# Kernel tuning notes

Hardware: AMD Instinct MI355X
Metric: run time of the kernel (lower is better)

The kernel has to match this reference:

```python
import jax, jax.numpy as jnp
import numpy as np

SCALE = 8.0  # sqrt(head_dim=64)


def setup_inputs() -> dict:
    key = jax.random.key(0)
    k1, k2, k3, k4 = jax.random.split(key, 4)
    B, Lq, Lk, H, C, K = 2, 4096, 4096, 8, 64, 32
    return {
        "query": jax.random.normal(k1, (B, Lq, H, C), dtype=jnp.float32),
        "key": jax.random.normal(k2, (B, Lk, H, C), dtype=jnp.float32),
        "value": jax.random.normal(k3, (B, Lk, H, C), dtype=jnp.float32),
        "pos": jax.random.randint(k4, (B, Lq, H, K), 0, Lk, dtype=jnp.int64),
    }


def reference(query, key, value, pos):
    # query: [B, Lq, H, C]; key/value: [B, Lk, H, C]; pos: [B, Lq, H, K]
    B, Lq, H, C = query.shape
    b_idx = jnp.arange(B)[:, None, None, None]   # [B,1,1,1]
    h_idx = jnp.arange(H)[None, None, :, None]   # [1,1,H,1]
    # gather along sequence dim per (batch, head): -> [B, Lq, H, K, C]
    k = key[b_idx, pos, h_idx, :]
    v = value[b_idx, pos, h_idx, :]
    # per-query attention over K gathered keys
    score = jnp.einsum("blhc,blhkc->blhk", query, k) / SCALE
    attn = jax.nn.softmax(score, axis=-1)
    out = jnp.einsum("blhk,blhkc->blhc", attn, v)
    return out
```

## Files before the change

### kernel.cpp

```cpp
#include <hip/hip_runtime.h>
#include <math.h>

constexpr int B  = 2;
constexpr int Lq = 4096;
constexpr int Lk = 4096;
constexpr int H  = 8;
constexpr int C  = 64;
constexpr int K  = 32;
constexpr float INV_SCALE = 0.125f;
constexpr int HC = H * C;
constexpr int NKV = B * Lk * H * C;

typedef _Float16 h2 __attribute__((ext_vector_type(2)));
typedef _Float16 half4_t __attribute__((ext_vector_type(4)));

static __device__ __forceinline__ h2 pack_h2(float lo, float hi) {
    return __builtin_bit_cast(h2, __builtin_amdgcn_cvt_pkrtz(lo, hi));
}

#if __has_builtin(__builtin_amdgcn_fdot2)
static __device__ __forceinline__ float fdot2(h2 a, h2 b, float c) {
    return __builtin_amdgcn_fdot2(a, b, c, false);
}
#else
static __device__ __forceinline__ float fdot2(h2 a, h2 b, float c) {
    return c + (float)a.x * (float)b.x + (float)a.y * (float)b.y;
}
#endif

static __device__ __forceinline__ h2 shfl_h2_xor(h2 v, int m) {
    int i = __builtin_bit_cast(int, v);
    i = __shfl_xor(i, m);
    return __builtin_bit_cast(h2, i);
}

template<int CTRL>
static __device__ __forceinline__ float dpp_f(float x) {
    return __builtin_bit_cast(float,
        __builtin_amdgcn_update_dpp(0, __builtin_bit_cast(int, x),
                                    CTRL, 0xF, 0xF, true));
}
template<int CTRL>
static __device__ __forceinline__ h2 dpp_h2(h2 x) {
    return __builtin_bit_cast(h2,
        __builtin_amdgcn_update_dpp(0, __builtin_bit_cast(int, x),
                                    CTRL, 0xF, 0xF, true));
}

__global__ __launch_bounds__(256) void convert_kv_f16(
    const float* __restrict__ key,
    const float* __restrict__ value,
    _Float16*    __restrict__ kh,
    _Float16*    __restrict__ vh)
{
    const int n4 = NKV / 4;
    for (int i = blockIdx.x * blockDim.x + threadIdx.x;
         i < 2 * n4; i += gridDim.x * blockDim.x) {
        if (i < n4) {
            const float4 v = ((const float4*)key)[i];
            half4_t h = { (_Float16)v.x, (_Float16)v.y, (_Float16)v.z, (_Float16)v.w };
            ((half4_t*)kh)[i] = h;
        } else {
            const float4 v = ((const float4*)value)[i - n4];
            half4_t h = { (_Float16)v.x, (_Float16)v.y, (_Float16)v.z, (_Float16)v.w };
            ((half4_t*)vh)[i - n4] = h;
        }
    }
}

__global__ __launch_bounds__(256, 2) void topk_attn_f16(
    const float*    __restrict__ query,
    const _Float16* __restrict__ keyh,
    const _Float16* __restrict__ valh,
    const int*      __restrict__ pos,
    float*          __restrict__ out)
{
    const int bid    = blockIdx.x;
    const int group  = bid & 15;
    const int lchunk = bid >> 4;
    const int wave   = threadIdx.x >> 6;
    const int lane   = threadIdx.x & 63;
    const int g      = lane >> 3;
    const int c8     = lane & 7;

    const int b = group >> 3;
    const int h = group & 7;
    const int l = lchunk * 4 + wave;

    const size_t row  = ((size_t)(b * Lq + l) * H + h);
    const size_t qoff = row * (size_t)C;

    const int4 pq = *(const int4*)(pos + row * (size_t)K + 4 * g);

    const _Float16* kbase = keyh + (size_t)b * Lk * HC + (size_t)h * C;
    const _Float16* vbase = valh + (size_t)b * Lk * HC + (size_t)h * C;

    int off[4];
    off[0] = pq.x * HC + 8 * c8;
    off[1] = pq.y * HC + 8 * c8;
    off[2] = pq.z * HC + 8 * c8;
    off[3] = pq.w * HC + 8 * c8;

    uint4 kv[4], vv[4];
    #pragma unroll
    for (int i = 0; i < 4; ++i) kv[i] = *(const uint4*)(kbase + off[i]);
    #pragma unroll
    for (int i = 0; i < 4; ++i) vv[i] = *(const uint4*)(vbase + off[i]);

    const float4 qa = *(const float4*)(query + qoff + 8 * c8);
    const float4 qb = *(const float4*)(query + qoff + 8 * c8 + 4);
    h2 qp[4];
    qp[0] = pack_h2(qa.x * INV_SCALE, qa.y * INV_SCALE);
    qp[1] = pack_h2(qa.z * INV_SCALE, qa.w * INV_SCALE);
    qp[2] = pack_h2(qb.x * INV_SCALE, qb.y * INV_SCALE);
    qp[3] = pack_h2(qb.z * INV_SCALE, qb.w * INV_SCALE);

    float s[4];
    #pragma unroll
    for (int i = 0; i < 4; ++i) {
        float t = fdot2(qp[0], __builtin_bit_cast(h2, kv[i].x), 0.0f);
        t = fdot2(qp[1], __builtin_bit_cast(h2, kv[i].y), t);
        t = fdot2(qp[2], __builtin_bit_cast(h2, kv[i].z), t);
        t = fdot2(qp[3], __builtin_bit_cast(h2, kv[i].w), t);
        t += dpp_f<0xB1>(t);
        t += dpp_f<0x4E>(t);
        t += dpp_f<0x141>(t);
        s[i] = t;
    }

    #pragma unroll
    for (int i = 0; i < 4; ++i) s[i] = __expf(s[i]);
    float se = (s[0] + s[1]) + (s[2] + s[3]);
    se += dpp_f<0x111>(se);
    se += dpp_f<0x112>(se);
    se += dpp_f<0x114>(se);
    se += dpp_f<0x118>(se);
    se += dpp_f<0x142>(se);
    se += dpp_f<0x143>(se);
    const float se_tot = __builtin_bit_cast(float,
        __builtin_amdgcn_readlane(__builtin_bit_cast(int, se), 63));
    const float inv = 8.0f / se_tot;

    h2 acc[4] = { h2{0,0}, h2{0,0}, h2{0,0}, h2{0,0} };
    #pragma unroll
    for (int i = 0; i < 4; ++i) {
        const float a = s[i] * inv;
        const h2 a2 = pack_h2(a, a);
        acc[0] = a2 * __builtin_bit_cast(h2, vv[i].x) + acc[0];
        acc[1] = a2 * __builtin_bit_cast(h2, vv[i].y) + acc[1];
        acc[2] = a2 * __builtin_bit_cast(h2, vv[i].z) + acc[2];
        acc[3] = a2 * __builtin_bit_cast(h2, vv[i].w) + acc[3];
    }
    #pragma unroll
    for (int j = 0; j < 4; ++j) acc[j] = acc[j] + dpp_h2<0x128>(acc[j]);
    #pragma unroll
    for (int j = 0; j < 4; ++j) acc[j] = acc[j] + shfl_h2_xor(acc[j], 16);
    #pragma unroll
    for (int j = 0; j < 4; ++j) acc[j] = acc[j] + shfl_h2_xor(acc[j], 32);

    if (g == 0) {
        const float4 o0 = make_float4((float)acc[0].x, (float)acc[0].y,
                                      (float)acc[1].x, (float)acc[1].y);
        const float4 o1 = make_float4((float)acc[2].x, (float)acc[2].y,
                                      (float)acc[3].x, (float)acc[3].y);
        *(float4*)(out + qoff + 8 * c8)     = o0;
        *(float4*)(out + qoff + 8 * c8 + 4) = o1;
    }
}

__global__ __launch_bounds__(256) void topk_attn_f32(
    const float* __restrict__ query,
    const float* __restrict__ key,
    const float* __restrict__ value,
    const int*   __restrict__ pos,
    float*       __restrict__ out)
{
    const int bid    = blockIdx.x;
    const int group  = bid & 15;
    const int lchunk = bid >> 4;
    const int wave   = threadIdx.x >> 6;
    const int lane   = threadIdx.x & 63;
    const int g      = lane >> 4;
    const int c4     = lane & 15;

    const int b = group >> 3;
    const int h = group & 7;
    const int l = lchunk * 4 + wave;

    const size_t row  = ((size_t)(b * Lq + l) * H + h);
    const size_t qoff = row * (size_t)C;

    float4 q4 = *(const float4*)(query + qoff + 4 * c4);
    q4.x *= INV_SCALE; q4.y *= INV_SCALE; q4.z *= INV_SCALE; q4.w *= INV_SCALE;

    const int p = pos[row * (size_t)K + (lane & 31)];

    const float* kbase = key   + (size_t)b * Lk * HC + (size_t)h * C;
    const float* vbase = value + (size_t)b * Lk * HC + (size_t)h * C;

    int off[8];
    #pragma unroll
    for (int i = 0; i < 8; ++i)
        off[i] = __shfl(p, 4 * i + g) * HC + 4 * c4;

    float s[8];
    #pragma unroll
    for (int i = 0; i < 8; ++i) {
        const float4 kv = *(const float4*)(kbase + off[i]);
        float t = q4.x * kv.x;
        t = fmaf(q4.y, kv.y, t);
        t = fmaf(q4.z, kv.z, t);
        t = fmaf(q4.w, kv.w, t);
        #pragma unroll
        for (int m = 8; m >= 1; m >>= 1) t += __shfl_xor(t, m);
        s[i] = t;
    }

    float mx = s[0];
    #pragma unroll
    for (int i = 1; i < 8; ++i) mx = fmaxf(mx, s[i]);
    mx = fmaxf(mx, __shfl_xor(mx, 16));
    mx = fmaxf(mx, __shfl_xor(mx, 32));

    float se = 0.0f;
    #pragma unroll
    for (int i = 0; i < 8; ++i) { s[i] = __expf(s[i] - mx); se += s[i]; }
    se += __shfl_xor(se, 16);
    se += __shfl_xor(se, 32);
    const float inv = 1.0f / se;

    float4 acc = make_float4(0.f, 0.f, 0.f, 0.f);
    #pragma unroll
    for (int i = 0; i < 8; ++i) {
        const float a = s[i] * inv;
        const float4 v4 = *(const float4*)(vbase + off[i]);
        acc.x = fmaf(a, v4.x, acc.x);
        acc.y = fmaf(a, v4.y, acc.y);
        acc.z = fmaf(a, v4.z, acc.z);
        acc.w = fmaf(a, v4.w, acc.w);
    }
    #pragma unroll
    for (int m = 16; m <= 32; m <<= 1) {
        acc.x += __shfl_xor(acc.x, m);
        acc.y += __shfl_xor(acc.y, m);
        acc.z += __shfl_xor(acc.z, m);
        acc.w += __shfl_xor(acc.w, m);
    }

    if (g == 0) *(float4*)(out + qoff + 4 * c4) = acc;
}

extern "C" void kernel_launch(void* const* d_in, const int* in_sizes, int n_in,
                              void* d_out, int out_size, void* d_ws, size_t ws_size,
                              hipStream_t stream) {
    const float* query = (const float*)d_in[0];
    const float* key   = (const float*)d_in[1];
    const float* value = (const float*)d_in[2];
    const int*   pos   = (const int*)d_in[3];
    float* out = (float*)d_out;

    const int total_rows = B * Lq * H;
    const int blocks = total_rows / 4;

    const size_t need = (size_t)2 * NKV * sizeof(_Float16);
    if (ws_size >= need && d_ws != nullptr) {
        _Float16* kh = (_Float16*)d_ws;
        _Float16* vh = kh + NKV;
        convert_kv_f16<<<2048, 256, 0, stream>>>(key, value, kh, vh);
        topk_attn_f16<<<blocks, 256, 0, stream>>>(query, kh, vh, pos, out);
    } else {
        topk_attn_f32<<<blocks, 256, 0, stream>>>(query, key, value, pos, out);
    }
}
```

Baseline: 45.86 us.

## Interleave fp16 K and V rows so each gather fetches one contiguous 256-byte row

The conversion kernel now writes K and V for each (batch, position, head) side by side in one fp16 row of 2*C halves, replacing two separate arrays. In the attention kernel, 16 lanes cover one combined K|V row, and each lane group handles 8 gathered positions instead of 4. The K-half lanes compute the scores and pass them to the V-half lanes through a DPP row broadcast, which drops the separate V-reduction DPP step. The goal is fewer, larger scattered memory transactions per gathered key. In exchange, half the lanes do wasted dot products, each thread holds more live registers, and the occupancy hint of 2 in the launch bounds is removed.

```diff
diff --git a/kernel.cpp b/kernel.cpp
--- a/kernel.cpp
+++ b/kernel.cpp
@@ -9,10 +9,11 @@
 constexpr int K  = 32;
 constexpr float INV_SCALE = 0.125f;
 constexpr int HC = H * C;
-constexpr int NKV = B * Lk * H * C;
+constexpr int NROWS = B * Lk * H;
+constexpr int KVROW = 2 * C;
 
 typedef _Float16 h2 __attribute__((ext_vector_type(2)));
-typedef _Float16 half4_t __attribute__((ext_vector_type(4)));
+typedef _Float16 half8 __attribute__((ext_vector_type(8)));
 
 static __device__ __forceinline__ h2 pack_h2(float lo, float hi) {
     return __builtin_bit_cast(h2, __builtin_amdgcn_cvt_pkrtz(lo, hi));
@@ -40,38 +41,29 @@
         __builtin_amdgcn_update_dpp(0, __builtin_bit_cast(int, x),
                                     CTRL, 0xF, 0xF, true));
 }
-template<int CTRL>
-static __device__ __forceinline__ h2 dpp_h2(h2 x) {
-    return __builtin_bit_cast(h2,
-        __builtin_amdgcn_update_dpp(0, __builtin_bit_cast(int, x),
-                                    CTRL, 0xF, 0xF, true));
-}
-
-__global__ __launch_bounds__(256) void convert_kv_f16(
+
+__global__ __launch_bounds__(256) void convert_kv_interleaved(
     const float* __restrict__ key,
     const float* __restrict__ value,
-    _Float16*    __restrict__ kh,
-    _Float16*    __restrict__ vh)
+    _Float16*    __restrict__ kvh)
 {
-    const int n4 = NKV / 4;
-    for (int i = blockIdx.x * blockDim.x + threadIdx.x;
-         i < 2 * n4; i += gridDim.x * blockDim.x) {
-        if (i < n4) {
-            const float4 v = ((const float4*)key)[i];
-            half4_t h = { (_Float16)v.x, (_Float16)v.y, (_Float16)v.z, (_Float16)v.w };
-            ((half4_t*)kh)[i] = h;
-        } else {
-            const float4 v = ((const float4*)value)[i - n4];
-            half4_t h = { (_Float16)v.x, (_Float16)v.y, (_Float16)v.z, (_Float16)v.w };
-            ((half4_t*)vh)[i - n4] = h;
-        }
-    }
-}
-
-__global__ __launch_bounds__(256, 2) void topk_attn_f16(
+    const int total = NROWS * 16;
+    for (int id = blockIdx.x * blockDim.x + threadIdx.x;
+         id < total; id += gridDim.x * blockDim.x) {
+        const int r = id >> 4;
+        const int j = id & 15;
+        const float* src = (j < 8 ? key : value) + (size_t)r * C + (j & 7) * 8;
+        const float4 a = *(const float4*)(src);
+        const float4 b = *(const float4*)(src + 4);
+        half8 o = { (_Float16)a.x, (_Float16)a.y, (_Float16)a.z, (_Float16)a.w,
+                    (_Float16)b.x, (_Float16)b.y, (_Float16)b.z, (_Float16)b.w };
+        *(half8*)(kvh + (size_t)r * KVROW + j * 8) = o;
+    }
+}
+
+__global__ __launch_bounds__(256) void topk_attn_kv16(
     const float*    __restrict__ query,
-    const _Float16* __restrict__ keyh,
-    const _Float16* __restrict__ valh,
+    const _Float16* __restrict__ kvh,
     const int*      __restrict__ pos,
     float*          __restrict__ out)
 {
@@ -80,8 +72,8 @@
     const int lchunk = bid >> 4;
     const int wave   = threadIdx.x >> 6;
     const int lane   = threadIdx.x & 63;
-    const int g      = lane >> 3;
-    const int c8     = lane & 7;
+    const int g      = lane >> 4;
+    const int c16    = lane & 15;
 
     const int b = group >> 3;
     const int h = group & 7;
@@ -90,47 +82,46 @@
     const size_t row  = ((size_t)(b * Lq + l) * H + h);
     const size_t qoff = row * (size_t)C;
 
-    const int4 pq = *(const int4*)(pos + row * (size_t)K + 4 * g);
-
-    const _Float16* kbase = keyh + (size_t)b * Lk * HC + (size_t)h * C;
-    const _Float16* vbase = valh + (size_t)b * Lk * HC + (size_t)h * C;
-
-    int off[4];
-    off[0] = pq.x * HC + 8 * c8;
-    off[1] = pq.y * HC + 8 * c8;
-    off[2] = pq.z * HC + 8 * c8;
-    off[3] = pq.w * HC + 8 * c8;
-
-    uint4 kv[4], vv[4];
-    #pragma unroll
-    for (int i = 0; i < 4; ++i) kv[i] = *(const uint4*)(kbase + off[i]);
-    #pragma unroll
-    for (int i = 0; i < 4; ++i) vv[i] = *(const uint4*)(vbase + off[i]);
-
-    const float4 qa = *(const float4*)(query + qoff + 8 * c8);
-    const float4 qb = *(const float4*)(query + qoff + 8 * c8 + 4);
+    const int* prow = pos + row * (size_t)K + 8 * g;
+    const int4 pq0 = *(const int4*)(prow);
+    const int4 pq1 = *(const int4*)(prow + 4);
+    const int pk[8] = { pq0.x, pq0.y, pq0.z, pq0.w,
+                        pq1.x, pq1.y, pq1.z, pq1.w };
+
+    const _Float16* kvbase = kvh + (size_t)b * Lk * H * KVROW
+                                 + (size_t)h * KVROW;
+
+    uint4 kvv[8];
+    #pragma unroll
+    for (int i = 0; i < 8; ++i)
+        kvv[i] = *(const uint4*)(kvbase + (size_t)pk[i] * (H * KVROW) + c16 * 8);
+
+    const float4 qa = *(const float4*)(query + qoff + 8 * (c16 & 7));
+    const float4 qb = *(const float4*)(query + qoff + 8 * (c16 & 7) + 4);
     h2 qp[4];
     qp[0] = pack_h2(qa.x * INV_SCALE, qa.y * INV_SCALE);
     qp[1] = pack_h2(qa.z * INV_SCALE, qa.w * INV_SCALE);
     qp[2] = pack_h2(qb.x * INV_SCALE, qb.y * INV_SCALE);
     qp[3] = pack_h2(qb.z * INV_SCALE, qb.w * INV_SCALE);
 
-    float s[4];
-    #pragma unroll
-    for (int i = 0; i < 4; ++i) {
-        float t = fdot2(qp[0], __builtin_bit_cast(h2, kv[i].x), 0.0f);
-        t = fdot2(qp[1], __builtin_bit_cast(h2, kv[i].y), t);
-        t = fdot2(qp[2], __builtin_bit_cast(h2, kv[i].z), t);
-        t = fdot2(qp[3], __builtin_bit_cast(h2, kv[i].w), t);
+    const bool is_k = (c16 < 8);
+
+    float s[8];
+    #pragma unroll
+    for (int i = 0; i < 8; ++i) {
+        float t = fdot2(qp[0], __builtin_bit_cast(h2, kvv[i].x), 0.0f);
+        t = fdot2(qp[1], __builtin_bit_cast(h2, kvv[i].y), t);
+        t = fdot2(qp[2], __builtin_bit_cast(h2, kvv[i].z), t);
+        t = fdot2(qp[3], __builtin_bit_cast(h2, kvv[i].w), t);
         t += dpp_f<0xB1>(t);
         t += dpp_f<0x4E>(t);
         t += dpp_f<0x141>(t);
-        s[i] = t;
-    }
-
-    #pragma unroll
-    for (int i = 0; i < 4; ++i) s[i] = __expf(s[i]);
-    float se = (s[0] + s[1]) + (s[2] + s[3]);
+        const float tr = dpp_f<0x128>(t);
+        t = is_k ? t : tr;
+        s[i] = __expf(t);
+    }
+
+    float se = ((s[0] + s[1]) + (s[2] + s[3])) + ((s[4] + s[5]) + (s[6] + s[7]));
     se += dpp_f<0x111>(se);
     se += dpp_f<0x112>(se);
     se += dpp_f<0x114>(se);
@@ -139,32 +130,31 @@
     se += dpp_f<0x143>(se);
     const float se_tot = __builtin_bit_cast(float,
         __builtin_amdgcn_readlane(__builtin_bit_cast(int, se), 63));
-    const float inv = 8.0f / se_tot;
+    const float inv = 16.0f / se_tot;
 
     h2 acc[4] = { h2{0,0}, h2{0,0}, h2{0,0}, h2{0,0} };
     #pragma unroll
-    for (int i = 0; i < 4; ++i) {
+    for (int i = 0; i < 8; ++i) {
         const float a = s[i] * inv;
         const h2 a2 = pack_h2(a, a);
-        acc[0] = a2 * __builtin_bit_cast(h2, vv[i].x) + acc[0];
-        acc[1] = a2 * __builtin_bit_cast(h2, vv[i].y) + acc[1];
-        acc[2] = a2 * __builtin_bit_cast(h2, vv[i].z) + acc[2];
-        acc[3] = a2 * __builtin_bit_cast(h2, vv[i].w) + acc[3];
-    }
-    #pragma unroll
-    for (int j = 0; j < 4; ++j) acc[j] = acc[j] + dpp_h2<0x128>(acc[j]);
+        acc[0] = a2 * __builtin_bit_cast(h2, kvv[i].x) + acc[0];
+        acc[1] = a2 * __builtin_bit_cast(h2, kvv[i].y) + acc[1];
+        acc[2] = a2 * __builtin_bit_cast(h2, kvv[i].z) + acc[2];
+        acc[3] = a2 * __builtin_bit_cast(h2, kvv[i].w) + acc[3];
+    }
     #pragma unroll
     for (int j = 0; j < 4; ++j) acc[j] = acc[j] + shfl_h2_xor(acc[j], 16);
     #pragma unroll
     for (int j = 0; j < 4; ++j) acc[j] = acc[j] + shfl_h2_xor(acc[j], 32);
 
-    if (g == 0) {
+    if (g == 0 && c16 >= 8) {
+        const int m = c16 - 8;
         const float4 o0 = make_float4((float)acc[0].x, (float)acc[0].y,
                                       (float)acc[1].x, (float)acc[1].y);
         const float4 o1 = make_float4((float)acc[2].x, (float)acc[2].y,
                                       (float)acc[3].x, (float)acc[3].y);
-        *(float4*)(out + qoff + 8 * c8)     = o0;
-        *(float4*)(out + qoff + 8 * c8 + 4) = o1;
+        *(float4*)(out + qoff + 8 * m)     = o0;
+        *(float4*)(out + qoff + 8 * m + 4) = o1;
     }
 }
 
@@ -262,12 +252,11 @@
     const int total_rows = B * Lq * H;
     const int blocks = total_rows / 4;
 
-    const size_t need = (size_t)2 * NKV * sizeof(_Float16);
+    const size_t need = (size_t)NROWS * KVROW * sizeof(_Float16);
     if (ws_size >= need && d_ws != nullptr) {
-        _Float16* kh = (_Float16*)d_ws;
-        _Float16* vh = kh + NKV;
-        convert_kv_f16<<<2048, 256, 0, stream>>>(key, value, kh, vh);
-        topk_attn_f16<<<blocks, 256, 0, stream>>>(query, kh, vh, pos, out);
+        _Float16* kvh = (_Float16*)d_ws;
+        convert_kv_interleaved<<<2048, 256, 0, stream>>>(key, value, kvh);
+        topk_attn_kv16<<<blocks, 256, 0, stream>>>(query, kvh, pos, out);
     } else {
         topk_attn_f32<<<blocks, 256, 0, stream>>>(query, key, value, pos, out);
     }
```

Result: no change. 45.74 us (-0.3%).
